# Kernel tuning notes

Hardware: AMD Instinct MI355X
Metric: run time of the kernel (lower is better)

The kernel has to match this reference:

```python
import jax, jax.numpy as jnp
import numpy as np

N, E, D, A, FC, B = 50000, 800000, 256, 7, 64, 512
EPS = 1e-5

def _glorot(key, fan_in, fan_out):
    lim = np.sqrt(6.0 / (fan_in + fan_out))
    return jax.random.uniform(key, (fan_in, fan_out), jnp.float32, -lim, lim)

def setup_inputs() -> dict:
    key = jax.random.key(0)
    ks = jax.random.split(key, 20)
    inp = {
        'x': jax.random.normal(ks[0], (N, 3), jnp.float32),
        'edge_index': jax.random.randint(ks[1], (2, E), 0, N, jnp.int32),
        'batch_index': jnp.sort(jax.random.randint(ks[2], (N,), 0, B, jnp.int32)),
        'a': jax.random.normal(ks[3], (B, A), jnp.float32),
        # GCNConv weights (lin weight + bias)
        'W0': _glorot(ks[4], 3, D),   'b0': jnp.zeros((D,), jnp.float32),
        'W1': _glorot(ks[5], D, D),   'b1': jnp.zeros((D,), jnp.float32),
        'W2': _glorot(ks[6], D, D),   'b2': jnp.zeros((D,), jnp.float32),
        'W3': _glorot(ks[7], D, D),   'b3': jnp.zeros((D,), jnp.float32),
        # action MLP
        'afc1_w': _glorot(ks[8], A, 8 * A),     'afc1_b': jnp.zeros((8 * A,), jnp.float32),
        'afc2_w': _glorot(ks[9], 8 * A, 8 * A), 'afc2_b': jnp.zeros((8 * A,), jnp.float32),
        'afc3_w': _glorot(ks[10], 8 * A, D),    'afc3_b': jnp.zeros((D,), jnp.float32),
        # head
        'fc1_w': _glorot(ks[11], D, FC), 'fc1_b': jnp.zeros((FC,), jnp.float32),
        'fc2_w': _glorot(ks[12], FC, 1), 'fc2_b': jnp.zeros((1,), jnp.float32),
        # LayerNorm affine params
        'ln1_g': jnp.ones((D,), jnp.float32),  'ln1_b': jnp.zeros((D,), jnp.float32),
        'ln2_g': jnp.ones((D,), jnp.float32),  'ln2_b': jnp.zeros((D,), jnp.float32),
        'ln4_g': jnp.ones((FC,), jnp.float32), 'ln4_b': jnp.zeros((FC,), jnp.float32),
        'ln5_g': jnp.ones((8 * A,), jnp.float32), 'ln5_b': jnp.zeros((8 * A,), jnp.float32),
    }
    return inp

def leaky(x):
    return jnp.where(x >= 0, x, 0.01 * x)

def layernorm(x, g, b):
    m = jnp.mean(x, axis=-1, keepdims=True)
    v = jnp.mean((x - m) ** 2, axis=-1, keepdims=True)
    return (x - m) * jax.lax.rsqrt(v + EPS) * g + b

def reference(x, edge_index, batch_index, a,
              W0, b0, W1, b1, W2, b2, W3, b3,
              afc1_w, afc1_b, afc2_w, afc2_b, afc3_w, afc3_b,
              fc1_w, fc1_b, fc2_w, fc2_b,
              ln1_g, ln1_b, ln2_g, ln2_b, ln4_g, ln4_b, ln5_g, ln5_b):
    n = x.shape[0]
    loop = jnp.arange(n, dtype=edge_index.dtype)
    src = jnp.concatenate([edge_index[0], loop])  # message sources
    dst = jnp.concatenate([edge_index[1], loop])  # message targets
    # symmetric GCN normalization with self-loops: deg over targets
    deg = jax.ops.segment_sum(jnp.ones_like(dst, dtype=x.dtype), dst, num_segments=n)
    dinv = jnp.where(deg > 0, jax.lax.rsqrt(deg), 0.0)
    norm = (dinv[src] * dinv[dst])[:, None]  # [E+N, 1]

    def gcn(h, W, bias):
        hw = h @ W
        agg = jax.ops.segment_sum(hw[src] * norm, dst, num_segments=n)
        return agg + bias

    h0 = gcn(x, W0, b0)
    h1 = leaky(gcn(h0, W1, b1)) + h0
    h2 = leaky(gcn(h1, W2, b2)) + h1
    h3 = leaky(gcn(h2, W3, b3)) + h2

    pooled = jax.ops.segment_max(h3, batch_index, num_segments=B)  # [B, D]
    V = layernorm(pooled, ln2_g, ln2_b)

    av = leaky(a @ afc1_w + afc1_b)
    av = layernorm(av, ln5_g, ln5_b)
    av = leaky(av @ afc2_w + afc2_b)
    av = leaky(av @ afc3_w + afc3_b)
    av = layernorm(av, ln1_g, ln1_b)

    z = V * av
    z = layernorm(leaky(z @ fc1_w + fc1_b), ln4_g, ln4_b)
    out = z @ fc2_w + fc2_b
    return out[:, 0]
```

## Files before the change

### kernel.cpp

```cpp
#include <hip/hip_runtime.h>

#define LN_EPS 1e-5f
#define SCAN_CHUNK 4096

typedef __bf16 bf16x8 __attribute__((ext_vector_type(8)));
typedef float f32x4 __attribute__((ext_vector_type(4)));
typedef float f32x2 __attribute__((ext_vector_type(2)));

__device__ __forceinline__ float b2f(unsigned short s) {
    union { unsigned u; float f; } c; c.u = ((unsigned)s) << 16; return c.f;
}
__device__ __forceinline__ unsigned short f2b(float f) {
    union { float f; unsigned u; } c; c.f = f;
    unsigned r = (c.u + 0x7FFFu + ((c.u >> 16) & 1u)) >> 16;
    return (unsigned short)r;
}
__device__ __forceinline__ f32x2 up2(unsigned u) {
    union { unsigned u; float f; } lo, hi;
    lo.u = u << 16; hi.u = u & 0xffff0000u;
    f32x2 r; r.x = lo.f; r.y = hi.f; return r;
}
__device__ __forceinline__ unsigned pk2(f32x2 v) {
    return ((unsigned)f2b(v.y) << 16) | (unsigned)f2b(v.x);
}
__device__ __forceinline__ float leaky(float x) { return x >= 0.f ? x : 0.01f * x; }
__device__ __forceinline__ unsigned encf(float f) {
    union { float f; unsigned u; } c; c.f = f;
    return ((int)c.u < 0) ? ~c.u : (c.u | 0x80000000u);
}
__device__ __forceinline__ float decf(unsigned u) {
    union { unsigned u; float f; } c;
    c.u = (u & 0x80000000u) ? (u & 0x7FFFFFFFu) : ~u;
    return c.f;
}


__global__ void init_kernel(int* ec, int* fill, int n) {
    int i = blockIdx.x * 256 + threadIdx.x;
    if (i < n) { ec[i] = 0; fill[i] = 0; }
}

__global__ void deg_kernel(const int* __restrict__ dst, int* ec, int e) {
    int i = blockIdx.x * 256 + threadIdx.x;
    if (i < e) atomicAdd(&ec[dst[i]], 1);
}

__global__ void scanA(const int* __restrict__ ec, int* __restrict__ bsum, int n) {
    __shared__ int red[4];
    int b = blockIdx.x, t = threadIdx.x;
    int base = b * SCAN_CHUNK + t * 16;
    int s = 0;
    #pragma unroll
    for (int k = 0; k < 16; ++k) { int i = base + k; if (i < n) s += (ec[i] + 7) & ~7; }
    #pragma unroll
    for (int off = 32; off; off >>= 1) s += __shfl_down(s, off, 64);
    if ((t & 63) == 0) red[t >> 6] = s;
    __syncthreads();
    if (t == 0) bsum[b] = red[0] + red[1] + red[2] + red[3];
}

__global__ void scanB(int* bsum, int nb) {
    if (threadIdx.x == 0) {
        int acc = 0;
        for (int i = 0; i < nb; ++i) { int v = bsum[i]; bsum[i] = acc; acc += v; }
        bsum[nb] = acc;
    }
}

__global__ void scanC(const int* __restrict__ ec, const int* __restrict__ bsum,
                      int* __restrict__ ptr, int n, int nb) {
    __shared__ int wsum[4];
    int b = blockIdx.x, t = threadIdx.x, lane = t & 63, w = t >> 6;
    int base = b * SCAN_CHUNK + t * 16;
    int loc[16]; int s = 0;
    #pragma unroll
    for (int k = 0; k < 16; ++k) {
        int i = base + k; int v = (i < n) ? ((ec[i] + 7) & ~7) : 0;
        loc[k] = s; s += v;
    }
    int x = s;
    #pragma unroll
    for (int off = 1; off < 64; off <<= 1) { int y = __shfl_up(x, off, 64); if (lane >= off) x += y; }
    if (lane == 63) wsum[w] = x;
    __syncthreads();
    int wexcl = 0;
    #pragma unroll
    for (int ww = 0; ww < 4; ++ww) if (ww < w) wexcl += wsum[ww];
    int toff = bsum[b] + wexcl + (x - s);
    #pragma unroll
    for (int k = 0; k < 16; ++k) { int i = base + k; if (i < n) ptr[i] = toff + loc[k]; }
    if (b == nb - 1 && t == 255) ptr[n] = bsum[nb];
}

__global__ void node_setup(const float* __restrict__ x, const int* __restrict__ ec,
                           const int* __restrict__ ptr,
                           float* __restrict__ dinv, float* __restrict__ sdeg,
                           float4* __restrict__ xp, int* __restrict__ csrc,
                           int n, int mpad) {
    int i = blockIdx.x * 256 + threadIdx.x;
    if (i >= mpad) return;
    float dv = 0.f, sv = 0.f;
    float4 v = make_float4(0.f, 0.f, 0.f, 0.f);
    if (i < n) {
        int e = ec[i];
        float dg = (float)(e + 1);
        dv = rsqrtf(dg); sv = sqrtf(dg);
        v.x = dv * x[i * 3]; v.y = dv * x[i * 3 + 1]; v.z = dv * x[i * 3 + 2];
        int p0 = ptr[i] + e, p1 = ptr[i] + ((e + 7) & ~7);
        int pad = n << 6;
        for (int j = p0; j < p1; ++j) csrc[j] = pad;
    }
    dinv[i] = dv; sdeg[i] = sv; xp[i] = v;
}

__global__ void fill_kernel(const int* __restrict__ src, const int* __restrict__ dst,
                            const int* __restrict__ ptr, int* fill,
                            int* __restrict__ csrc, int e) {
    int i = blockIdx.x * 256 + threadIdx.x;
    if (i < e) {
        int d = dst[i];
        int pos = atomicAdd(&fill[d], 1);
        csrc[ptr[d] + pos] = src[i] << 6;
    }
}


__global__ void wt_kernel(const float* __restrict__ W1, const float* __restrict__ W2,
                          const float* __restrict__ W3, unsigned short* __restrict__ wt) {
    int k = blockIdx.x, l = blockIdx.y, nn = threadIdx.x;
    const float* W = (l == 0) ? W1 : (l == 1) ? W2 : W3;
    wt[l * 65536 + nn * 256 + k] = f2b(W[k * 256 + nn]);
}


__global__ void aggx_kernel(const float4* __restrict__ xp, const float* __restrict__ dinv,
                            const int* __restrict__ ptr, const int* __restrict__ csrc,
                            float* __restrict__ aggx, int n) {
    int i = blockIdx.x * 256 + threadIdx.x;
    if (i >= n) return;
    const char* xb = (const char*)xp;
    float4 self = xp[i];
    float a0 = self.x, a1 = self.y, a2 = self.z;
    float p0 = 0.f, p1 = 0.f, p2 = 0.f;
    float q0 = 0.f, q1 = 0.f, q2 = 0.f;
    float r0 = 0.f, r1 = 0.f, r2 = 0.f;
    int e0 = ptr[i], e1 = ptr[i + 1];
    for (int e = e0; e < e1; e += 4) {
        int4 v = *(const int4*)(csrc + e);
        float4 u0 = *(const float4*)(xb + (((unsigned)v.x) >> 2));
        float4 u1 = *(const float4*)(xb + (((unsigned)v.y) >> 2));
        float4 u2 = *(const float4*)(xb + (((unsigned)v.z) >> 2));
        float4 u3 = *(const float4*)(xb + (((unsigned)v.w) >> 2));
        a0 += u0.x; a1 += u0.y; a2 += u0.z;
        p0 += u1.x; p1 += u1.y; p2 += u1.z;
        q0 += u2.x; q1 += u2.y; q2 += u2.z;
        r0 += u3.x; r1 += u3.y; r2 += u3.z;
    }
    a0 += (p0 + q0) + r0; a1 += (p1 + q1) + r1; a2 += (p2 + q2) + r2;
    float di = dinv[i];
    aggx[i * 3] = a0 * di; aggx[i * 3 + 1] = a1 * di; aggx[i * 3 + 2] = a2 * di;
}

__global__ __launch_bounds__(256) void h0_kernel(const float* __restrict__ aggx,
                          const float* __restrict__ W0, const float* __restrict__ b0,
                          const float* __restrict__ dinv,
                          unsigned short* __restrict__ hbs,
                          int n, int mpad) {
    int t = threadIdx.x;
    int row = blockIdx.x * 4 + (t >> 6);
    int f = (t & 63) * 4;
    if (row >= mpad) return;
    unsigned short* hp = hbs + ((size_t)(f >> 5) * mpad + row) * 32 + (f & 31);
    if (row < n) {
        float a0 = aggx[row * 3], a1 = aggx[row * 3 + 1], a2 = aggx[row * 3 + 2];
        float4 w0 = *(const float4*)(W0 + f);
        float4 w1 = *(const float4*)(W0 + 256 + f);
        float4 w2 = *(const float4*)(W0 + 512 + f);
        float4 bb = *(const float4*)(b0 + f);
        float4 v;
        v.x = bb.x + a0 * w0.x + a1 * w1.x + a2 * w2.x;
        v.y = bb.y + a0 * w0.y + a1 * w1.y + a2 * w2.y;
        v.z = bb.z + a0 * w0.z + a1 * w1.z + a2 * w2.z;
        v.w = bb.w + a0 * w0.w + a1 * w1.w + a2 * w2.w;
        float di = dinv[row];
        ushort4 o;
        o.x = f2b(di * v.x); o.y = f2b(di * v.y); o.z = f2b(di * v.z); o.w = f2b(di * v.w);
        *(ushort4*)hp = o;
    } else {
        ushort4 o; o.x = 0; o.y = 0; o.z = 0; o.w = 0;
        *(ushort4*)hp = o;
    }
}


__global__ __launch_bounds__(256) void spmm_kernel(
    const unsigned short* __restrict__ hbs,
    const int* __restrict__ ptr, const int* __restrict__ csrc,
    const float* __restrict__ dinv,
    unsigned short* __restrict__ agg,
    int n, int mpad) {
    int chunk = blockIdx.x & 7;
    int g = blockIdx.x >> 3;
    int t = threadIdx.x;
    int node = g * 64 + (t >> 2);
    if (node >= n) return;
    unsigned loff = (unsigned)((t & 3) << 4);
    const char* cb = (const char*)hbs + (size_t)chunk * mpad * 64;
    int e0 = ptr[node], e1 = ptr[node + 1];
    uint4 own = *(const uint4*)(cb + (((unsigned)node << 6) | loff));
    f32x2 accA0 = up2(own.x), accA1 = up2(own.y), accA2 = up2(own.z), accA3 = up2(own.w);
    f32x2 accB0 = (f32x2)(0.f), accB1 = (f32x2)(0.f), accB2 = (f32x2)(0.f), accB3 = (f32x2)(0.f);
    int e = e0;
    int4 ia, ib;
    if (e < e1) { ia = *(const int4*)(csrc + e); ib = *(const int4*)(csrc + e + 4); }
    while (e < e1) {
        int en = e + 8;
        int4 na, nb;
        if (en < e1) { na = *(const int4*)(csrc + en); nb = *(const int4*)(csrc + en + 4); }
        uint4 u0 = *(const uint4*)(cb + ((unsigned)ia.x | loff));
        uint4 u1 = *(const uint4*)(cb + ((unsigned)ia.y | loff));
        uint4 u2 = *(const uint4*)(cb + ((unsigned)ia.z | loff));
        uint4 u3 = *(const uint4*)(cb + ((unsigned)ia.w | loff));
        uint4 u4 = *(const uint4*)(cb + ((unsigned)ib.x | loff));
        uint4 u5 = *(const uint4*)(cb + ((unsigned)ib.y | loff));
        uint4 u6 = *(const uint4*)(cb + ((unsigned)ib.z | loff));
        uint4 u7 = *(const uint4*)(cb + ((unsigned)ib.w | loff));
        accA0 += up2(u0.x); accA1 += up2(u0.y); accA2 += up2(u0.z); accA3 += up2(u0.w);
        accB0 += up2(u1.x); accB1 += up2(u1.y); accB2 += up2(u1.z); accB3 += up2(u1.w);
        accA0 += up2(u2.x); accA1 += up2(u2.y); accA2 += up2(u2.z); accA3 += up2(u2.w);
        accB0 += up2(u3.x); accB1 += up2(u3.y); accB2 += up2(u3.z); accB3 += up2(u3.w);
        accA0 += up2(u4.x); accA1 += up2(u4.y); accA2 += up2(u4.z); accA3 += up2(u4.w);
        accB0 += up2(u5.x); accB1 += up2(u5.y); accB2 += up2(u5.z); accB3 += up2(u5.w);
        accA0 += up2(u6.x); accA1 += up2(u6.y); accA2 += up2(u6.z); accA3 += up2(u6.w);
        accB0 += up2(u7.x); accB1 += up2(u7.y); accB2 += up2(u7.z); accB3 += up2(u7.w);
        ia = na; ib = nb; e = en;
    }
    float di = dinv[node];
    f32x2 dd; dd.x = di; dd.y = di;
    accA0 = (accA0 + accB0) * dd;
    accA1 = (accA1 + accB1) * dd;
    accA2 = (accA2 + accB2) * dd;
    accA3 = (accA3 + accB3) * dd;
    uint4 o;
    o.x = pk2(accA0); o.y = pk2(accA1); o.z = pk2(accA2); o.w = pk2(accA3);
    *(uint4*)((char*)agg + (size_t)chunk * mpad * 64 + (((unsigned)node << 6) | loff)) = o;
}


__global__ __launch_bounds__(256) void gemm_kernel(const unsigned short* __restrict__ A,
                                                   const unsigned short* __restrict__ Bt,
                                                   const float* __restrict__ bias,
                                                   const float* __restrict__ dinv,
                                                   const float* __restrict__ sdeg,
                                                   unsigned short* __restrict__ hbs,
                                                   const int* __restrict__ batch,
                                                   unsigned* __restrict__ pooledu,
                                                   int mpad, int n, int last) {
    const int K = 256;
    __shared__ int sb[32];
    int wid = threadIdx.x >> 6, lane = threadIdx.x & 63;
    int m0 = blockIdx.x * 32;
    if (last && threadIdx.x < 32) {
        int r = m0 + threadIdx.x;
        sb[threadIdx.x] = (r < n) ? batch[r] : -1;
    }
    if (last) __syncthreads();
    int n0 = wid * 64;
    int lr = lane & 15, lg = lane >> 4;
    f32x4 acc[2][4];
    #pragma unroll
    for (int i = 0; i < 2; i++)
        #pragma unroll
        for (int j = 0; j < 4; j++) acc[i][j] = (f32x4)(0.f);
    const unsigned short* Ap = A + ((size_t)(m0 + lr)) * 32 + lg * 8;
    const unsigned short* Bp = Bt + (size_t)(n0 + lr) * K + lg * 8;
    if (!last) {
        #pragma unroll
        for (int kc = 0; kc < 8; ++kc) {
            bf16x8 af[2], bfr[4];
            #pragma unroll
            for (int mi = 0; mi < 2; mi++)
                af[mi] = *(const bf16x8*)(Ap + (size_t)kc * mpad * 32 + mi * 512);
            #pragma unroll
            for (int ni = 0; ni < 4; ni++)
                bfr[ni] = *(const bf16x8*)(Bp + (size_t)ni * 16 * K + kc * 32);
            #pragma unroll
            for (int mi = 0; mi < 2; mi++)
                #pragma unroll
                for (int ni = 0; ni < 4; ni++)
                    acc[mi][ni] = __builtin_amdgcn_mfma_f32_16x16x32_bf16(bfr[ni], af[mi], acc[mi][ni], 0, 0, 0);
        }
        #pragma unroll
        for (int mi = 0; mi < 2; mi++) {
            int r = m0 + mi * 16 + lr;
            float dv = dinv[r];
            float sv = sdeg[r];
            #pragma unroll
            for (int ni = 0; ni < 4; ni++) {
                int c0 = n0 + ni * 16 + lg * 4;
                float4 bb = *(const float4*)(bias + c0);
                int ch = c0 >> 5, cf = c0 & 31;
                unsigned short* hp = hbs + ((size_t)ch * mpad + r) * 32 + cf;
                ushort4 hv = *(const ushort4*)hp;
                float v0 = leaky(acc[mi][ni][0] + bb.x) + b2f(hv.x) * sv;
                float v1 = leaky(acc[mi][ni][1] + bb.y) + b2f(hv.y) * sv;
                float v2 = leaky(acc[mi][ni][2] + bb.z) + b2f(hv.z) * sv;
                float v3 = leaky(acc[mi][ni][3] + bb.w) + b2f(hv.w) * sv;
                ushort4 o;
                o.x = f2b(v0 * dv); o.y = f2b(v1 * dv); o.z = f2b(v2 * dv); o.w = f2b(v3 * dv);
                *(ushort4*)hp = o;
            }
        }
    } else {
        #pragma unroll
        for (int kc = 0; kc < 8; ++kc) {
            bf16x8 af[2], bfr[4];
            #pragma unroll
            for (int mi = 0; mi < 2; mi++)
                af[mi] = *(const bf16x8*)(Ap + (size_t)kc * mpad * 32 + mi * 512);
            #pragma unroll
            for (int ni = 0; ni < 4; ni++)
                bfr[ni] = *(const bf16x8*)(Bp + (size_t)ni * 16 * K + kc * 32);
            #pragma unroll
            for (int mi = 0; mi < 2; mi++)
                #pragma unroll
                for (int ni = 0; ni < 4; ni++)
                    acc[mi][ni] = __builtin_amdgcn_mfma_f32_16x16x32_bf16(af[mi], bfr[ni], acc[mi][ni], 0, 0, 0);
        }
        #pragma unroll
        for (int ni = 0; ni < 4; ni++) {
            int c = n0 + ni * 16 + lr;
            float bv = bias[c];
            int ch = c >> 5, cf = c & 31;
            const unsigned short* hpb = hbs + (size_t)ch * mpad * 32 + cf;
            int cs = -1; float cm = 0.f;
            #pragma unroll
            for (int mi = 0; mi < 2; mi++) {
                int rb = mi * 16 + lg * 4;
                #pragma unroll
                for (int j = 0; j < 4; ++j) {
                    int row = m0 + rb + j;
                    int seg = sb[rb + j];
                    float ho = b2f(hpb[(size_t)row * 32]) * sdeg[row];
                    float v = leaky(acc[mi][ni][j] + bv) + ho;
                    if (seg >= 0) {
                        if (seg != cs) {
                            if (cs >= 0) atomicMax(pooledu + (size_t)cs * 256 + c, encf(cm));
                            cs = seg; cm = v;
                        } else {
                            cm = fmaxf(cm, v);
                        }
                    }
                }
            }
            if (cs >= 0) atomicMax(pooledu + (size_t)cs * 256 + c, encf(cm));
        }
    }
}

__global__ void pool_init_kernel(unsigned* pooledu) {
    pooledu[blockIdx.x * 256 + threadIdx.x] = 0u;
}


__device__ __forceinline__ float blk_sum(float v, float* red) {
    #pragma unroll
    for (int off = 32; off; off >>= 1) v += __shfl_down(v, off, 64);
    int lane = threadIdx.x & 63, wid = threadIdx.x >> 6;
    if (lane == 0) red[wid] = v;
    __syncthreads();
    float s = red[0] + red[1] + red[2] + red[3];
    __syncthreads();
    return s;
}

__global__ __launch_bounds__(256) void head_kernel(
    const unsigned* __restrict__ pooledu, const float* __restrict__ a,
    const float* __restrict__ afc1_w, const float* __restrict__ afc1_b,
    const float* __restrict__ afc2_w, const float* __restrict__ afc2_b,
    const float* __restrict__ afc3_w, const float* __restrict__ afc3_b,
    const float* __restrict__ fc1_w, const float* __restrict__ fc1_b,
    const float* __restrict__ fc2_w, const float* __restrict__ fc2_b,
    const float* __restrict__ ln1_g, const float* __restrict__ ln1_b,
    const float* __restrict__ ln2_g, const float* __restrict__ ln2_b,
    const float* __restrict__ ln4_g, const float* __restrict__ ln4_b,
    const float* __restrict__ ln5_g, const float* __restrict__ ln5_b,
    float* __restrict__ out) {
    __shared__ float red[4];
    __shared__ float sM[2];
    __shared__ float s1[56], s2[56], sZ[256], sT[64];
    int b = blockIdx.x, tid = threadIdx.x;

    float pv = decf(pooledu[(size_t)b * 256 + tid]);
    float m = blk_sum(pv, red) * (1.f / 256.f);
    float d0 = pv - m;
    float var = blk_sum(d0 * d0, red) * (1.f / 256.f);
    float V = d0 * rsqrtf(var + LN_EPS) * ln2_g[tid] + ln2_b[tid];

    if (tid < 56) {
        float acc = afc1_b[tid];
        #pragma unroll
        for (int k = 0; k < 7; ++k) acc += a[b * 7 + k] * afc1_w[k * 56 + tid];
        s1[tid] = leaky(acc);
    }
    __syncthreads();
    if (tid == 0) {
        float s = 0.f; for (int k = 0; k < 56; ++k) s += s1[k];
        float mm = s / 56.f;
        float q = 0.f; for (int k = 0; k < 56; ++k) { float d = s1[k] - mm; q += d * d; }
        sM[0] = mm; sM[1] = rsqrtf(q / 56.f + LN_EPS);
    }
    __syncthreads();
    if (tid < 56) s1[tid] = (s1[tid] - sM[0]) * sM[1] * ln5_g[tid] + ln5_b[tid];
    __syncthreads();
    if (tid < 56) {
        float acc = afc2_b[tid];
        for (int k = 0; k < 56; ++k) acc += s1[k] * afc2_w[k * 56 + tid];
        s2[tid] = leaky(acc);
    }
    __syncthreads();
    float acc = afc3_b[tid];
    for (int k = 0; k < 56; ++k) acc += s2[k] * afc3_w[k * 256 + tid];
    acc = leaky(acc);
    m = blk_sum(acc, red) * (1.f / 256.f);
    d0 = acc - m;
    var = blk_sum(d0 * d0, red) * (1.f / 256.f);
    float av = d0 * rsqrtf(var + LN_EPS) * ln1_g[tid] + ln1_b[tid];

    float z = V * av;
    sZ[tid] = z;
    __syncthreads();
    if (tid < 64) {
        float a2 = fc1_b[tid];
        for (int k = 0; k < 256; ++k) a2 += sZ[k] * fc1_w[k * 64 + tid];
        sT[tid] = leaky(a2);
    }
    __syncthreads();
    if (tid == 0) {
        float s = 0.f; for (int k = 0; k < 64; ++k) s += sT[k];
        float mm = s / 64.f;
        float q = 0.f; for (int k = 0; k < 64; ++k) { float d = sT[k] - mm; q += d * d; }
        float r = rsqrtf(q / 64.f + LN_EPS);
        float o = fc2_b[0];
        for (int k = 0; k < 64; ++k) {
            float zz = (sT[k] - mm) * r * ln4_g[k] + ln4_b[k];
            o += zz * fc2_w[k];
        }
        out[b] = o;
    }
}


extern "C" void kernel_launch(void* const* d_in, const int* in_sizes, int n_in,
                              void* d_out, int out_size, void* d_ws, size_t ws_size,
                              hipStream_t stream) {
    const float* x     = (const float*)d_in[0];
    const int*   eidx  = (const int*)d_in[1];
    const int*   batch = (const int*)d_in[2];
    const float* a     = (const float*)d_in[3];
    const float* W0 = (const float*)d_in[4];  const float* b0 = (const float*)d_in[5];
    const float* W1 = (const float*)d_in[6];  const float* b1 = (const float*)d_in[7];
    const float* W2 = (const float*)d_in[8];  const float* b2 = (const float*)d_in[9];
    const float* W3 = (const float*)d_in[10]; const float* b3 = (const float*)d_in[11];
    const float* afc1_w = (const float*)d_in[12]; const float* afc1_b = (const float*)d_in[13];
    const float* afc2_w = (const float*)d_in[14]; const float* afc2_b = (const float*)d_in[15];
    const float* afc3_w = (const float*)d_in[16]; const float* afc3_b = (const float*)d_in[17];
    const float* fc1_w  = (const float*)d_in[18]; const float* fc1_b  = (const float*)d_in[19];
    const float* fc2_w  = (const float*)d_in[20]; const float* fc2_b  = (const float*)d_in[21];
    const float* ln1_g = (const float*)d_in[22]; const float* ln1_b = (const float*)d_in[23];
    const float* ln2_g = (const float*)d_in[24]; const float* ln2_b = (const float*)d_in[25];
    const float* ln4_g = (const float*)d_in[26]; const float* ln4_b = (const float*)d_in[27];
    const float* ln5_g = (const float*)d_in[28]; const float* ln5_b = (const float*)d_in[29];

    int N = in_sizes[0] / 3;
    int E = in_sizes[1] / 2;
    int B = in_sizes[3] / 7;
    int Mpad = ((N + 63) / 64) * 64;
    int NB = (N + SCAN_CHUNK - 1) / SCAN_CHUNK;
    int Ecap = E + 7 * N + 8;

    char* p = (char*)d_ws;
    auto alloc = [&](size_t bytes) -> char* {
        char* r = p; p += (bytes + 255) & ~(size_t)255; return r;
    };
    int*   ec   = (int*)alloc((size_t)N * 4);
    int*   fill = (int*)alloc((size_t)N * 4);
    int*   ptr  = (int*)alloc((size_t)(N + 1) * 4);
    int*   bsum = (int*)alloc((size_t)(NB + 1) * 4);
    int*   csrc = (int*)alloc((size_t)Ecap * 4);
    float* dinv = (float*)alloc((size_t)Mpad * 4);
    float* sdeg = (float*)alloc((size_t)Mpad * 4);
    float4* xp  = (float4*)alloc((size_t)Mpad * 16);
    float* aggx = (float*)alloc((size_t)N * 3 * 4);
    unsigned short* hbs = (unsigned short*)alloc((size_t)Mpad * 256 * 2);
    unsigned short* agg = (unsigned short*)alloc((size_t)Mpad * 256 * 2);
    unsigned short* wt  = (unsigned short*)alloc((size_t)3 * 65536 * 2);
    unsigned* pooledu = (unsigned*)alloc((size_t)B * 256 * 4);

    const int* srcl = eidx;
    const int* dstl = eidx + E;

    init_kernel<<<(N + 255) / 256, 256, 0, stream>>>(ec, fill, N);
    deg_kernel<<<(E + 255) / 256, 256, 0, stream>>>(dstl, ec, E);
    scanA<<<NB, 256, 0, stream>>>(ec, bsum, N);
    scanB<<<1, 64, 0, stream>>>(bsum, NB);
    scanC<<<NB, 256, 0, stream>>>(ec, bsum, ptr, N, NB);
    node_setup<<<(Mpad + 255) / 256, 256, 0, stream>>>(x, ec, ptr, dinv, sdeg, xp, csrc, N, Mpad);
    fill_kernel<<<(E + 255) / 256, 256, 0, stream>>>(srcl, dstl, ptr, fill, csrc, E);
    wt_kernel<<<dim3(256, 3), 256, 0, stream>>>(W1, W2, W3, wt);
    aggx_kernel<<<(N + 255) / 256, 256, 0, stream>>>(xp, dinv, ptr, csrc, aggx, N);
    h0_kernel<<<Mpad / 4, 256, 0, stream>>>(aggx, W0, b0, dinv, hbs, N, Mpad);
    pool_init_kernel<<<B, 256, 0, stream>>>(pooledu);

    const float* biases[3] = { b1, b2, b3 };
    int nblkN = (N + 63) / 64;
    for (int l = 0; l < 3; ++l) {
        spmm_kernel<<<nblkN * 8, 256, 0, stream>>>(hbs, ptr, csrc, dinv, agg, N, Mpad);
        gemm_kernel<<<Mpad / 32, 256, 0, stream>>>(agg, wt + (size_t)l * 65536, biases[l],
                                                   dinv, sdeg, hbs, batch, pooledu,
                                                   Mpad, N, (l == 2) ? 1 : 0);
    }

    head_kernel<<<B, 256, 0, stream>>>(pooledu, a,
        afc1_w, afc1_b, afc2_w, afc2_b, afc3_w, afc3_b,
        fc1_w, fc1_b, fc2_w, fc2_b,
        ln1_g, ln1_b, ln2_g, ln2_b, ln4_g, ln4_b, ln5_g, ln5_b,
        (float*)d_out);
}
```

Baseline: 537.3 us.

## Fuse SpMM aggregation into GEMM layer kernel with row-major ping-pong buffers

Merges the per-layer sparse aggregation and the dense MFMA GEMM into one kernel. Each block aggregates its 32 rows into shared memory, then runs the GEMM and epilogue from there. This removes the intermediate agg buffer round-trip and one launch per layer. Activations switch from a 32-column chunked layout to plain row-major, with ping-pong input and output buffers, and the edge indices are rescaled to 512-byte row strides. In exchange, a wave now gathers a full 512-byte row per neighbor instead of eight chunked blocks sharing cache locality. Per-block aggregation may also be unbalanced and limit occupancy because of the shared-memory tile.

```diff
diff --git a/kernel.cpp b/kernel.cpp
--- a/kernel.cpp
+++ b/kernel.cpp
@@ -107,7 +107,7 @@
         dv = rsqrtf(dg); sv = sqrtf(dg);
         v.x = dv * x[i * 3]; v.y = dv * x[i * 3 + 1]; v.z = dv * x[i * 3 + 2];
         int p0 = ptr[i] + e, p1 = ptr[i] + ((e + 7) & ~7);
-        int pad = n << 6;
+        int pad = n << 9;
         for (int j = p0; j < p1; ++j) csrc[j] = pad;
     }
     dinv[i] = dv; sdeg[i] = sv; xp[i] = v;
@@ -120,7 +120,7 @@
     if (i < e) {
         int d = dst[i];
         int pos = atomicAdd(&fill[d], 1);
-        csrc[ptr[d] + pos] = src[i] << 6;
+        csrc[ptr[d] + pos] = src[i] << 9;
     }
 }
 
@@ -147,10 +147,10 @@
     int e0 = ptr[i], e1 = ptr[i + 1];
     for (int e = e0; e < e1; e += 4) {
         int4 v = *(const int4*)(csrc + e);
-        float4 u0 = *(const float4*)(xb + (((unsigned)v.x) >> 2));
-        float4 u1 = *(const float4*)(xb + (((unsigned)v.y) >> 2));
-        float4 u2 = *(const float4*)(xb + (((unsigned)v.z) >> 2));
-        float4 u3 = *(const float4*)(xb + (((unsigned)v.w) >> 2));
+        float4 u0 = *(const float4*)(xb + (((unsigned)v.x) >> 5));
+        float4 u1 = *(const float4*)(xb + (((unsigned)v.y) >> 5));
+        float4 u2 = *(const float4*)(xb + (((unsigned)v.z) >> 5));
+        float4 u3 = *(const float4*)(xb + (((unsigned)v.w) >> 5));
         a0 += u0.x; a1 += u0.y; a2 += u0.z;
         p0 += u1.x; p1 += u1.y; p2 += u1.z;
         q0 += u2.x; q1 += u2.y; q2 += u2.z;
@@ -170,7 +170,7 @@
     int row = blockIdx.x * 4 + (t >> 6);
     int f = (t & 63) * 4;
     if (row >= mpad) return;
-    unsigned short* hp = hbs + ((size_t)(f >> 5) * mpad + row) * 32 + (f & 31);
+    unsigned short* hp = hbs + (size_t)row * 256 + f;
     if (row < n) {
         float a0 = aggx[row * 3], a1 = aggx[row * 3 + 1], a2 = aggx[row * 3 + 2];
         float4 w0 = *(const float4*)(W0 + f);
@@ -193,78 +193,74 @@
 }
 
 
-__global__ __launch_bounds__(256) void spmm_kernel(
-    const unsigned short* __restrict__ hbs,
+__global__ __launch_bounds__(256) void layer_kernel(
+    const unsigned short* __restrict__ hin,
+    const unsigned short* __restrict__ Bt,
+    const float* __restrict__ bias,
+    const float* __restrict__ dinv, const float* __restrict__ sdeg,
+    unsigned short* __restrict__ hout,
     const int* __restrict__ ptr, const int* __restrict__ csrc,
-    const float* __restrict__ dinv,
-    unsigned short* __restrict__ agg,
-    int n, int mpad) {
-    int chunk = blockIdx.x & 7;
-    int g = blockIdx.x >> 3;
-    int t = threadIdx.x;
-    int node = g * 64 + (t >> 2);
-    if (node >= n) return;
-    unsigned loff = (unsigned)((t & 3) << 4);
-    const char* cb = (const char*)hbs + (size_t)chunk * mpad * 64;
-    int e0 = ptr[node], e1 = ptr[node + 1];
-    uint4 own = *(const uint4*)(cb + (((unsigned)node << 6) | loff));
-    f32x2 accA0 = up2(own.x), accA1 = up2(own.y), accA2 = up2(own.z), accA3 = up2(own.w);
-    f32x2 accB0 = (f32x2)(0.f), accB1 = (f32x2)(0.f), accB2 = (f32x2)(0.f), accB3 = (f32x2)(0.f);
-    int e = e0;
-    int4 ia, ib;
-    if (e < e1) { ia = *(const int4*)(csrc + e); ib = *(const int4*)(csrc + e + 4); }
-    while (e < e1) {
-        int en = e + 8;
-        int4 na, nb;
-        if (en < e1) { na = *(const int4*)(csrc + en); nb = *(const int4*)(csrc + en + 4); }
-        uint4 u0 = *(const uint4*)(cb + ((unsigned)ia.x | loff));
-        uint4 u1 = *(const uint4*)(cb + ((unsigned)ia.y | loff));
-        uint4 u2 = *(const uint4*)(cb + ((unsigned)ia.z | loff));
-        uint4 u3 = *(const uint4*)(cb + ((unsigned)ia.w | loff));
-        uint4 u4 = *(const uint4*)(cb + ((unsigned)ib.x | loff));
-        uint4 u5 = *(const uint4*)(cb + ((unsigned)ib.y | loff));
-        uint4 u6 = *(const uint4*)(cb + ((unsigned)ib.z | loff));
-        uint4 u7 = *(const uint4*)(cb + ((unsigned)ib.w | loff));
-        accA0 += up2(u0.x); accA1 += up2(u0.y); accA2 += up2(u0.z); accA3 += up2(u0.w);
-        accB0 += up2(u1.x); accB1 += up2(u1.y); accB2 += up2(u1.z); accB3 += up2(u1.w);
-        accA0 += up2(u2.x); accA1 += up2(u2.y); accA2 += up2(u2.z); accA3 += up2(u2.w);
-        accB0 += up2(u3.x); accB1 += up2(u3.y); accB2 += up2(u3.z); accB3 += up2(u3.w);
-        accA0 += up2(u4.x); accA1 += up2(u4.y); accA2 += up2(u4.z); accA3 += up2(u4.w);
-        accB0 += up2(u5.x); accB1 += up2(u5.y); accB2 += up2(u5.z); accB3 += up2(u5.w);
-        accA0 += up2(u6.x); accA1 += up2(u6.y); accA2 += up2(u6.z); accA3 += up2(u6.w);
-        accB0 += up2(u7.x); accB1 += up2(u7.y); accB2 += up2(u7.z); accB3 += up2(u7.w);
-        ia = na; ib = nb; e = en;
-    }
-    float di = dinv[node];
-    f32x2 dd; dd.x = di; dd.y = di;
-    accA0 = (accA0 + accB0) * dd;
-    accA1 = (accA1 + accB1) * dd;
-    accA2 = (accA2 + accB2) * dd;
-    accA3 = (accA3 + accB3) * dd;
-    uint4 o;
-    o.x = pk2(accA0); o.y = pk2(accA1); o.z = pk2(accA2); o.w = pk2(accA3);
-    *(uint4*)((char*)agg + (size_t)chunk * mpad * 64 + (((unsigned)node << 6) | loff)) = o;
-}
-
-
-__global__ __launch_bounds__(256) void gemm_kernel(const unsigned short* __restrict__ A,
-                                                   const unsigned short* __restrict__ Bt,
-                                                   const float* __restrict__ bias,
-                                                   const float* __restrict__ dinv,
-                                                   const float* __restrict__ sdeg,
-                                                   unsigned short* __restrict__ hbs,
-                                                   const int* __restrict__ batch,
-                                                   unsigned* __restrict__ pooledu,
-                                                   int mpad, int n, int last) {
+    const int* __restrict__ batch, unsigned* __restrict__ pooledu,
+    int mpad, int n, int last) {
     const int K = 256;
+    const int PITCH = 528;
+    __shared__ unsigned short At[32 * 264];
     __shared__ int sb[32];
-    int wid = threadIdx.x >> 6, lane = threadIdx.x & 63;
+    int tid = threadIdx.x;
+    int wid = tid >> 6, lane = tid & 63;
     int m0 = blockIdx.x * 32;
-    if (last && threadIdx.x < 32) {
-        int r = m0 + threadIdx.x;
-        sb[threadIdx.x] = (r < n) ? batch[r] : -1;
-    }
-    if (last) __syncthreads();
+    int half = lane >> 5, l = lane & 31;
+    unsigned loff = (unsigned)(l << 4);
+    const char* hb = (const char*)hin;
+
+    for (int pair = 0; pair < 4; ++pair) {
+        int rl = wid * 8 + pair * 2 + half;
+        int node = m0 + rl;
+        uint4 o4 = make_uint4(0u, 0u, 0u, 0u);
+        if (node < n) {
+            uint4 own = *(const uint4*)(hb + (((unsigned)node) << 9) + loff);
+            f32x2 a0 = up2(own.x), a1 = up2(own.y), a2 = up2(own.z), a3 = up2(own.w);
+            f32x2 c0 = (f32x2)(0.f), c1 = (f32x2)(0.f), c2 = (f32x2)(0.f), c3 = (f32x2)(0.f);
+            int e0 = ptr[node], e1 = ptr[node + 1];
+            int e = e0;
+            int4 ia, ib;
+            if (e < e1) { ia = *(const int4*)(csrc + e); ib = *(const int4*)(csrc + e + 4); }
+            while (e < e1) {
+                int en = e + 8;
+                int4 na, nb;
+                if (en < e1) { na = *(const int4*)(csrc + en); nb = *(const int4*)(csrc + en + 4); }
+                uint4 u0 = *(const uint4*)(hb + (unsigned)ia.x + loff);
+                uint4 u1 = *(const uint4*)(hb + (unsigned)ia.y + loff);
+                uint4 u2 = *(const uint4*)(hb + (unsigned)ia.z + loff);
+                uint4 u3 = *(const uint4*)(hb + (unsigned)ia.w + loff);
+                uint4 u4 = *(const uint4*)(hb + (unsigned)ib.x + loff);
+                uint4 u5 = *(const uint4*)(hb + (unsigned)ib.y + loff);
+                uint4 u6 = *(const uint4*)(hb + (unsigned)ib.z + loff);
+                uint4 u7 = *(const uint4*)(hb + (unsigned)ib.w + loff);
+                a0 += up2(u0.x); a1 += up2(u0.y); a2 += up2(u0.z); a3 += up2(u0.w);
+                c0 += up2(u1.x); c1 += up2(u1.y); c2 += up2(u1.z); c3 += up2(u1.w);
+                a0 += up2(u2.x); a1 += up2(u2.y); a2 += up2(u2.z); a3 += up2(u2.w);
+                c0 += up2(u3.x); c1 += up2(u3.y); c2 += up2(u3.z); c3 += up2(u3.w);
+                a0 += up2(u4.x); a1 += up2(u4.y); a2 += up2(u4.z); a3 += up2(u4.w);
+                c0 += up2(u5.x); c1 += up2(u5.y); c2 += up2(u5.z); c3 += up2(u5.w);
+                a0 += up2(u6.x); a1 += up2(u6.y); a2 += up2(u6.z); a3 += up2(u6.w);
+                c0 += up2(u7.x); c1 += up2(u7.y); c2 += up2(u7.z); c3 += up2(u7.w);
+                ia = na; ib = nb; e = en;
+            }
+            float di = dinv[node];
+            f32x2 dd; dd.x = di; dd.y = di;
+            a0 = (a0 + c0) * dd; a1 = (a1 + c1) * dd;
+            a2 = (a2 + c2) * dd; a3 = (a3 + c3) * dd;
+            o4.x = pk2(a0); o4.y = pk2(a1); o4.z = pk2(a2); o4.w = pk2(a3);
+        }
+        *(uint4*)((char*)At + rl * PITCH + loff) = o4;
+    }
+    if (last && tid < 32) {
+        int r = m0 + tid;
+        sb[tid] = (r < n) ? batch[r] : -1;
+    }
+    __syncthreads();
+
     int n0 = wid * 64;
     int lr = lane & 15, lg = lane >> 4;
     f32x4 acc[2][4];
@@ -272,7 +268,7 @@
     for (int i = 0; i < 2; i++)
         #pragma unroll
         for (int j = 0; j < 4; j++) acc[i][j] = (f32x4)(0.f);
-    const unsigned short* Ap = A + ((size_t)(m0 + lr)) * 32 + lg * 8;
+    const char* Ab = (const char*)At;
     const unsigned short* Bp = Bt + (size_t)(n0 + lr) * K + lg * 8;
     if (!last) {
         #pragma unroll
@@ -280,7 +276,7 @@
             bf16x8 af[2], bfr[4];
             #pragma unroll
             for (int mi = 0; mi < 2; mi++)
-                af[mi] = *(const bf16x8*)(Ap + (size_t)kc * mpad * 32 + mi * 512);
+                af[mi] = *(const bf16x8*)(Ab + (mi * 16 + lr) * PITCH + kc * 64 + lg * 16);
             #pragma unroll
             for (int ni = 0; ni < 4; ni++)
                 bfr[ni] = *(const bf16x8*)(Bp + (size_t)ni * 16 * K + kc * 32);
@@ -298,17 +294,21 @@
             #pragma unroll
             for (int ni = 0; ni < 4; ni++) {
                 int c0 = n0 + ni * 16 + lg * 4;
-                float4 bb = *(const float4*)(bias + c0);
-                int ch = c0 >> 5, cf = c0 & 31;
-                unsigned short* hp = hbs + ((size_t)ch * mpad + r) * 32 + cf;
-                ushort4 hv = *(const ushort4*)hp;
-                float v0 = leaky(acc[mi][ni][0] + bb.x) + b2f(hv.x) * sv;
-                float v1 = leaky(acc[mi][ni][1] + bb.y) + b2f(hv.y) * sv;
-                float v2 = leaky(acc[mi][ni][2] + bb.z) + b2f(hv.z) * sv;
-                float v3 = leaky(acc[mi][ni][3] + bb.w) + b2f(hv.w) * sv;
-                ushort4 o;
-                o.x = f2b(v0 * dv); o.y = f2b(v1 * dv); o.z = f2b(v2 * dv); o.w = f2b(v3 * dv);
-                *(ushort4*)hp = o;
+                unsigned short* hp = hout + (size_t)r * 256 + c0;
+                if (r < n) {
+                    float4 bb = *(const float4*)(bias + c0);
+                    ushort4 hv = *(const ushort4*)(hin + (size_t)r * 256 + c0);
+                    float v0 = leaky(acc[mi][ni][0] + bb.x) + b2f(hv.x) * sv;
+                    float v1 = leaky(acc[mi][ni][1] + bb.y) + b2f(hv.y) * sv;
+                    float v2 = leaky(acc[mi][ni][2] + bb.z) + b2f(hv.z) * sv;
+                    float v3 = leaky(acc[mi][ni][3] + bb.w) + b2f(hv.w) * sv;
+                    ushort4 o;
+                    o.x = f2b(v0 * dv); o.y = f2b(v1 * dv); o.z = f2b(v2 * dv); o.w = f2b(v3 * dv);
+                    *(ushort4*)hp = o;
+                } else {
+                    ushort4 o; o.x = 0; o.y = 0; o.z = 0; o.w = 0;
+                    *(ushort4*)hp = o;
+                }
             }
         }
     } else {
@@ -317,7 +317,7 @@
             bf16x8 af[2], bfr[4];
             #pragma unroll
             for (int mi = 0; mi < 2; mi++)
-                af[mi] = *(const bf16x8*)(Ap + (size_t)kc * mpad * 32 + mi * 512);
+                af[mi] = *(const bf16x8*)(Ab + (mi * 16 + lr) * PITCH + kc * 64 + lg * 16);
             #pragma unroll
             for (int ni = 0; ni < 4; ni++)
                 bfr[ni] = *(const bf16x8*)(Bp + (size_t)ni * 16 * K + kc * 32);
@@ -327,12 +327,22 @@
                 for (int ni = 0; ni < 4; ni++)
                     acc[mi][ni] = __builtin_amdgcn_mfma_f32_16x16x32_bf16(af[mi], bfr[ni], acc[mi][ni], 0, 0, 0);
         }
+        unsigned short hres[4][2][4];
+        #pragma unroll
+        for (int ni = 0; ni < 4; ni++) {
+            int c = n0 + ni * 16 + lr;
+            #pragma unroll
+            for (int mi = 0; mi < 2; mi++)
+                #pragma unroll
+                for (int j = 0; j < 4; ++j) {
+                    int row = m0 + mi * 16 + lg * 4 + j;
+                    hres[ni][mi][j] = hin[(size_t)row * 256 + c];
+                }
+        }
         #pragma unroll
         for (int ni = 0; ni < 4; ni++) {
             int c = n0 + ni * 16 + lr;
             float bv = bias[c];
-            int ch = c >> 5, cf = c & 31;
-            const unsigned short* hpb = hbs + (size_t)ch * mpad * 32 + cf;
             int cs = -1; float cm = 0.f;
             #pragma unroll
             for (int mi = 0; mi < 2; mi++) {
@@ -341,7 +351,7 @@
                 for (int j = 0; j < 4; ++j) {
                     int row = m0 + rb + j;
                     int seg = sb[rb + j];
-                    float ho = b2f(hpb[(size_t)row * 32]) * sdeg[row];
+                    float ho = b2f(hres[ni][mi][j]) * sdeg[row];
                     float v = leaky(acc[mi][ni][j] + bv) + ho;
                     if (seg >= 0) {
                         if (seg != cs) {
@@ -492,8 +502,8 @@
     float* sdeg = (float*)alloc((size_t)Mpad * 4);
     float4* xp  = (float4*)alloc((size_t)Mpad * 16);
     float* aggx = (float*)alloc((size_t)N * 3 * 4);
-    unsigned short* hbs = (unsigned short*)alloc((size_t)Mpad * 256 * 2);
-    unsigned short* agg = (unsigned short*)alloc((size_t)Mpad * 256 * 2);
+    unsigned short* hbs0 = (unsigned short*)alloc((size_t)Mpad * 256 * 2);
+    unsigned short* hbs1 = (unsigned short*)alloc((size_t)Mpad * 256 * 2);
     unsigned short* wt  = (unsigned short*)alloc((size_t)3 * 65536 * 2);
     unsigned* pooledu = (unsigned*)alloc((size_t)B * 256 * 4);
 
@@ -509,17 +519,16 @@
     fill_kernel<<<(E + 255) / 256, 256, 0, stream>>>(srcl, dstl, ptr, fill, csrc, E);
     wt_kernel<<<dim3(256, 3), 256, 0, stream>>>(W1, W2, W3, wt);
     aggx_kernel<<<(N + 255) / 256, 256, 0, stream>>>(xp, dinv, ptr, csrc, aggx, N);
-    h0_kernel<<<Mpad / 4, 256, 0, stream>>>(aggx, W0, b0, dinv, hbs, N, Mpad);
+    h0_kernel<<<Mpad / 4, 256, 0, stream>>>(aggx, W0, b0, dinv, hbs0, N, Mpad);
     pool_init_kernel<<<B, 256, 0, stream>>>(pooledu);
 
-    const float* biases[3] = { b1, b2, b3 };
-    int nblkN = (N + 63) / 64;
-    for (int l = 0; l < 3; ++l) {
-        spmm_kernel<<<nblkN * 8, 256, 0, stream>>>(hbs, ptr, csrc, dinv, agg, N, Mpad);
-        gemm_kernel<<<Mpad / 32, 256, 0, stream>>>(agg, wt + (size_t)l * 65536, biases[l],
-                                                   dinv, sdeg, hbs, batch, pooledu,
-                                                   Mpad, N, (l == 2) ? 1 : 0);
-    }
+    int nblk = Mpad / 32;
+    layer_kernel<<<nblk, 256, 0, stream>>>(hbs0, wt,           b1, dinv, sdeg, hbs1,
+                                           ptr, csrc, batch, pooledu, Mpad, N, 0);
+    layer_kernel<<<nblk, 256, 0, stream>>>(hbs1, wt + 65536,   b2, dinv, sdeg, hbs0,
+                                           ptr, csrc, batch, pooledu, Mpad, N, 0);
+    layer_kernel<<<nblk, 256, 0, stream>>>(hbs0, wt + 131072,  b3, dinv, sdeg, hbs1,
+                                           ptr, csrc, batch, pooledu, Mpad, N, 1);
 
     head_kernel<<<B, 256, 0, stream>>>(pooledu, a,
         afc1_w, afc1_b, afc2_w, afc2_b, afc3_w, afc3_b,
```

Result: no change. 527.1 us (-1.9%).
